# Performance work log

Hardware: AMD Instinct MI355X
Metric: run time of the kernel (lower is better)

## Reference

```python
import jax, jax.numpy as jnp
from jax import lax
import numpy as np

# Module hyperparameters (init_kwargs)
NITERS = 10
NROWS, NCOLS = 16, 16
NSUP = NROWS * NCOLS
COMPACT = 10.0
CONST = 100.0
NCONV = 10  # stage1_nconv; also nfeat of imfeat and shifter_size
B, H, W = 2, 512, 512

DN = ('NCHW', 'OIHW', 'NCHW')


def conv2d(x, w, b=None):
    y = lax.conv_general_dilated(x, w, (1, 1), 'SAME', dimension_numbers=DN)
    return y if b is None else y + b[None, :, None, None]


def blockmean(x):
    # adaptive_avg_pool2d to (NROWS, NCOLS); H,W chosen divisible -> exact block mean
    Bz, C, Hx, Wx = x.shape
    return x.reshape(Bz, C, NROWS, Hx // NROWS, NCOLS, Wx // NCOLS).mean((3, 5))


def box3(x):
    # 3x3 all-ones depthwise conv with zero padding (the "shifter" conv)
    C = x.shape[1]
    k = jnp.ones((C, 1, 3, 3), x.dtype)
    return lax.conv_general_dilated(x, k, (1, 1), 'SAME', feature_group_count=C,
                                    dimension_numbers=DN)


def setup_inputs() -> dict:
    key = jax.random.key(0)
    ks = jax.random.split(key, 7)
    s = 0.15  # ~He init for 3x3 convs with ~10 channels; keeps activations O(1)
    return {
        'X': jax.random.normal(ks[0], (B, 3, H, W), jnp.float32),
        'w0': jax.random.normal(ks[1], (NCONV, 3, 3, 3), jnp.float32) * s,
        'b0': jax.random.normal(ks[2], (NCONV,), jnp.float32) * s,
        'ws_mid': jax.random.normal(ks[3], (NCONV - 2, NCONV, NCONV, 3, 3), jnp.float32) * s,
        'bs_mid': jax.random.normal(ks[4], (NCONV - 2, NCONV), jnp.float32) * s,
        'wf': jax.random.normal(ks[5], (NCONV - 5, NCONV, 3, 3), jnp.float32) * s,
        'bf': jax.random.normal(ks[6], (NCONV - 5,), jnp.float32) * s,
    }


def _forward(X, w0, b0, ws_mid, bs_mid, wf, bf):
    Bz, _, Hx, Wx = X.shape
    h = jax.nn.relu(conv2d(X, w0, b0))

    def layer(hc, wb):
        w, b = wb
        return jax.nn.relu(conv2d(hc, w, b)), None

    h, _ = lax.scan(layer, h, (ws_mid, bs_mid))
    s1 = conv2d(h, wf, bf)  # B x (NCONV-5) x H x W

    # ---- imfeat = [stage1, X, Xgrid, Ygrid] -> B x NCONV x H x W ----
    Yg, Xg = jnp.meshgrid(jnp.arange(Hx, dtype=X.dtype), jnp.arange(Wx, dtype=X.dtype),
                          indexing='ij')
    imfeat = jnp.concatenate([
        s1, X,
        jnp.broadcast_to(Xg, (Bz, 1, Hx, Wx)),
        jnp.broadcast_to(Yg, (Bz, 1, Hx, Wx)),
    ], axis=1)
    C = imfeat.shape[1]

    # ckern: ones, except spatial (last two) channels weighted by compactness scale
    ck = jnp.ones((C,), imfeat.dtype).at[-2:].set(
        jnp.asarray(COMPACT / np.sqrt(Hx * Wx / NSUP), imfeat.dtype))

    # pixel -> parent superpixel indices (nearest-neighbor upsample of coarse grid)
    Yc = jnp.arange(Hx) * NROWS // Hx  # (H,)
    Xc = jnp.arange(Wx) * NCOLS // Wx  # (W,)
    shifts = [(dr, dc) for dr in (-1, 0, 1) for dc in (-1, 0, 1)]
    Y1 = jnp.stack([jnp.clip(Yc + dr, 0, NROWS - 1) for dr, _ in shifts])[:, :, None]  # (9,H,1)
    X1 = jnp.stack([jnp.clip(Xc + dc, 0, NCOLS - 1) for _, dc in shifts])[:, None, :]  # (9,1,W)

    def affinity_fn(cent):
        cup = cent[:, :, Y1, X1]
        d = (imfeat[:, :, None] - cup) * ck[None, :, None, None, None]
        return jnp.exp(-(d * d).mean(1) / CONST)

    def centroids_fn(aff):
        # sum over the 9 shifts commutes with block-mean and the shared 3x3 box conv
        asum = aff.sum(1, keepdims=True)
        num = box3(blockmean(imfeat * asum))  # B x C x NROWS x NCOLS
        den = box3(blockmean(asum))
        return num / den

    cent0 = blockmean(imfeat)
    aff0 = affinity_fn(cent0)

    @jax.checkpoint
    def step(carry, _):
        cent, _a = carry
        aff = affinity_fn(cent)
        return (centroids_fn(aff), aff), None

    (cent, aff), _ = lax.scan(step, (cent0, aff0), None, length=NITERS)
    # returned affinity corresponds to centroids before the last update (as in torch)
    return cent, aff


def reference(X, w0, b0, ws_mid, bs_mid, wf, bf):
    return _forward(X, w0, b0, ws_mid, bs_mid, wf, bf)
```

## Files before the change

kernel.cpp:

```cpp
#include <hip/hip_runtime.h>

#define HH 512
#define WW 512
#define BB 2
#define CKXY 0.3125f
#define HW (HH*WW)

typedef short bf16x8 __attribute__((ext_vector_type(8)));
typedef float f32x4  __attribute__((ext_vector_type(4)));

__device__ __forceinline__ unsigned short f2bf(float f) {
  unsigned u = __float_as_uint(f);
  u += 0x7FFF + ((u >> 16) & 1);
  return (unsigned short)(u >> 16);
}

__global__ __launch_bounds__(512) void conv_mfma(const float* __restrict__ in,
    const float* __restrict__ w, const float* __restrict__ bias,
    float* __restrict__ out) {
  const int bx = blockIdx.x, by = blockIdx.y, b = blockIdx.z;
  const int tid = threadIdx.x;
  const int gy0 = by * 32, gx0 = bx * 32;
  __shared__ unsigned short sT[34 * 34 * 16];
  const float* inb = in + (size_t)b * 10 * HW;

  const int lane = tid & 63;
  const int g = lane >> 4;
  const int co = lane & 15;
  bf16x8 Bf[5];
  #pragma unroll
  for (int P = 0; P < 5; ++P) {
    #pragma unroll
    for (int j = 0; j < 8; ++j) {
      const int tap = 2 * P + (g >> 1);
      const int ci = ((g & 1) << 3) + j;
      unsigned short v = 0;
      if (co < 10 && ci < 10 && tap < 9)
        v = f2bf(w[(co * 10 + ci) * 9 + tap]);
      Bf[P][j] = (short)v;
    }
  }
  const float bs = (co < 10) ? bias[co] : 0.f;

  for (int p = tid; p < 34 * 34; p += 512) {
    const int ly = p / 34, lx = p - ly * 34;
    const int gy = gy0 + ly - 1, gx = gx0 + lx - 1;
    const bool ok = ((unsigned)gy < HH) && ((unsigned)gx < WW);
    const float* pp = inb + gy * WW + gx;
    unsigned u[5];
    #pragma unroll
    for (int c2 = 0; c2 < 5; ++c2) {
      float f0 = ok ? pp[(2 * c2) * HW] : 0.f;
      float f1 = ok ? pp[(2 * c2 + 1) * HW] : 0.f;
      u[c2] = (unsigned)f2bf(f0) | ((unsigned)f2bf(f1) << 16);
    }
    uint4* dst = reinterpret_cast<uint4*>(&sT[p * 16]);
    dst[0] = make_uint4(u[0], u[1], u[2], u[3]);
    dst[1] = make_uint4(u[4], 0u, 0u, 0u);
  }
  __syncthreads();

  const int wave = tid >> 6;
  float* outb = out + (size_t)b * 10 * HW;
  for (int i = 0; i < 8; ++i) {
    const int t = wave * 8 + i;
    const int py = t >> 1;
    const int pxb = (t & 1) << 4;
    f32x4 acc = {bs, bs, bs, bs};
    #pragma unroll
    for (int P = 0; P < 5; ++P) {
      int tap = 2 * P + (g >> 1);
      if (tap > 8) tap = 8;
      const int dy = tap / 3 - 1, dx = tap % 3 - 1;
      const int m = lane & 15;
      const int addr = ((py + 1 + dy) * 34 + (pxb + m + 1 + dx)) * 16 + ((g & 1) << 3);
      bf16x8 a = *reinterpret_cast<const bf16x8*>(&sT[addr]);
      acc = __builtin_amdgcn_mfma_f32_16x16x32_bf16(a, Bf[P], acc, 0, 0, 0);
    }
    if (co < 10) {
      const int y = gy0 + py;
      const int x = gx0 + pxb + (g << 2);
      float4 o;
      o.x = fmaxf(acc[0], 0.f);
      o.y = fmaxf(acc[1], 0.f);
      o.z = fmaxf(acc[2], 0.f);
      o.w = fmaxf(acc[3], 0.f);
      *reinterpret_cast<float4*>(&outb[co * HW + y * WW + x]) = o;
    }
  }
}

template<int CIN, int COUT, bool RELU>
__global__ __launch_bounds__(1024) void conv3x3_t32(const float* __restrict__ in,
    const float* __restrict__ w, const float* __restrict__ bias,
    float* __restrict__ out) {
  const int bx = blockIdx.x, by = blockIdx.y, b = blockIdx.z;
  const int tid = threadIdx.x;
  const int xl = tid & 31, yl = tid >> 5;
  __shared__ float sIn[CIN][34][40];
  const float* inb = in + (size_t)b * CIN * HW;
  const int gy0 = by * 32, gx0 = bx * 32;
  #pragma unroll
  for (int ci = 0; ci < CIN; ++ci)
    sIn[ci][yl + 1][xl + 1] = inb[ci * HW + (gy0 + yl) * WW + gx0 + xl];
  for (int idx = tid; idx < CIN * 132; idx += 1024) {
    int ci = idx / 132, rem = idx - ci * 132;
    int ly, lx;
    if (rem < 34)       { ly = 0;  lx = rem; }
    else if (rem < 68)  { ly = 33; lx = rem - 34; }
    else if (rem < 100) { lx = 0;  ly = rem - 68 + 1; }
    else                { lx = 33; ly = rem - 100 + 1; }
    int gy = gy0 + ly - 1, gx = gx0 + lx - 1;
    float v = 0.f;
    if ((unsigned)gy < HH && (unsigned)gx < WW) v = inb[ci * HW + gy * WW + gx];
    sIn[ci][ly][lx] = v;
  }
  __syncthreads();

  float acc[COUT];
  #pragma unroll
  for (int co = 0; co < COUT; ++co) acc[co] = bias[co];
  #pragma unroll
  for (int ci = 0; ci < CIN; ++ci) {
    float v[9];
    #pragma unroll
    for (int t = 0; t < 9; ++t) v[t] = sIn[ci][yl + t / 3][xl + t % 3];
    #pragma unroll
    for (int co = 0; co < COUT; ++co) {
      #pragma unroll
      for (int t = 0; t < 9; ++t)
        acc[co] = fmaf(v[t], w[(co * CIN + ci) * 9 + t], acc[co]);
    }
  }
  float* outb = out + (size_t)b * COUT * HW;
  const int p = (gy0 + yl) * WW + gx0 + xl;
  #pragma unroll
  for (int co = 0; co < COUT; ++co) {
    float r = RELU ? fmaxf(acc[co], 0.f) : acc[co];
    outb[co * HW + p] = r;
  }
}

__global__ __launch_bounds__(1024) void conv_final_t32(const float* __restrict__ in,
    const float* __restrict__ w, const float* __restrict__ bias,
    const float* __restrict__ X, float* __restrict__ imfeat,
    float* __restrict__ cent0) {
  const int bx = blockIdx.x, by = blockIdx.y, b = blockIdx.z;
  const int tid = threadIdx.x;
  const int xl = tid & 31, yl = tid >> 5;
  __shared__ float sIn[10][34][40];
  const float* inb = in + (size_t)b * 10 * HW;
  const int gy0 = by * 32, gx0 = bx * 32;
  #pragma unroll
  for (int ci = 0; ci < 10; ++ci)
    sIn[ci][yl + 1][xl + 1] = inb[ci * HW + (gy0 + yl) * WW + gx0 + xl];
  for (int idx = tid; idx < 10 * 132; idx += 1024) {
    int ci = idx / 132, rem = idx - ci * 132;
    int ly, lx;
    if (rem < 34)       { ly = 0;  lx = rem; }
    else if (rem < 68)  { ly = 33; lx = rem - 34; }
    else if (rem < 100) { lx = 0;  ly = rem - 68 + 1; }
    else                { lx = 33; ly = rem - 100 + 1; }
    int gy = gy0 + ly - 1, gx = gx0 + lx - 1;
    float v = 0.f;
    if ((unsigned)gy < HH && (unsigned)gx < WW) v = inb[ci * HW + gy * WW + gx];
    sIn[ci][ly][lx] = v;
  }
  __syncthreads();

  float acc[5];
  #pragma unroll
  for (int co = 0; co < 5; ++co) acc[co] = bias[co];
  #pragma unroll
  for (int ci = 0; ci < 10; ++ci) {
    float v[9];
    #pragma unroll
    for (int t = 0; t < 9; ++t) v[t] = sIn[ci][yl + t / 3][xl + t % 3];
    #pragma unroll
    for (int co = 0; co < 5; ++co) {
      #pragma unroll
      for (int t = 0; t < 9; ++t)
        acc[co] = fmaf(v[t], w[(co * 10 + ci) * 9 + t], acc[co]);
    }
  }
  float* ob = imfeat + (size_t)b * 10 * HW;
  const float* Xb = X + (size_t)b * 3 * HW;
  const int y = gy0 + yl, x = gx0 + xl;
  const int p = y * WW + x;
  float cs[10];
  #pragma unroll
  for (int co = 0; co < 5; ++co) { float v = acc[co]; ob[co * HW + p] = v; cs[co] = v; }
  #pragma unroll
  for (int c = 0; c < 3; ++c) { float v = Xb[c * HW + p]; ob[(5 + c) * HW + p] = v; cs[5 + c] = v; }
  float xc = (float)x * CKXY, yc = (float)y * CKXY;
  ob[8 * HW + p] = xc; cs[8] = xc;
  ob[9 * HW + p] = yc; cs[9] = yc;
  #pragma unroll
  for (int off = 32; off; off >>= 1) {
    #pragma unroll
    for (int ch = 0; ch < 10; ++ch) cs[ch] += __shfl_down(cs[ch], off);
  }
  __shared__ float sP[16][10];
  const int wave = tid >> 6;
  if ((tid & 63) == 0) {
    #pragma unroll
    for (int ch = 0; ch < 10; ++ch) sP[wave][ch] = cs[ch];
  }
  __syncthreads();
  if (tid < 10) {
    float s = 0.f;
    #pragma unroll
    for (int wv = 0; wv < 16; ++wv) s += sP[wv][tid];
    cent0[((b * 10 + tid) * 16 + by) * 16 + bx] = s * (1.0f / 1024.0f);
  }
}

__global__ __launch_bounds__(256) void iter2(const float* __restrict__ imfeat,
    const float* __restrict__ centIn, const float* __restrict__ numP,
    const float* __restrict__ denP, float* __restrict__ numO,
    float* __restrict__ denO, float* __restrict__ affO) {
  const int cx = blockIdx.x, cy = blockIdx.y, b = blockIdx.z;
  const int tid = threadIdx.x;
  __shared__ float sc[9][10];
  __shared__ float nb[9][11];
  if (centIn) {
    if (tid < 90) {
      int s = tid / 10, ch = tid - s * 10;
      int dr = s / 3 - 1, dc = s % 3 - 1;
      int r = min(max(cy + dr, 0), 15), c = min(max(cx + dc, 0), 15);
      sc[s][ch] = centIn[((b * 10 + ch) * 16 + r) * 16 + c];
    }
    __syncthreads();
  } else {
    if (tid < 99) {
      int s = tid / 11, j = tid - s * 11;
      int dr = s / 3 - 1, dc = s % 3 - 1;
      int r = min(max(cy + dr, 0), 15), c = min(max(cx + dc, 0), 15);
      float a = 0.f;
      #pragma unroll
      for (int rr = -1; rr <= 1; ++rr)
        #pragma unroll
        for (int cc = -1; cc <= 1; ++cc) {
          int R = r + rr, C = c + cc;
          if ((unsigned)R < 16u && (unsigned)C < 16u)
            a += (j < 10) ? numP[((b * 10 + j) * 16 + R) * 16 + C]
                          : denP[(b * 16 + R) * 16 + C];
        }
      nb[s][j] = a;
    }
    __syncthreads();
    if (tid < 90) {
      int s = tid / 10, ch = tid - s * 10;
      sc[s][ch] = nb[s][ch] / nb[s][10];
    }
    __syncthreads();
  }

  float accN[10];
  #pragma unroll
  for (int ch = 0; ch < 10; ++ch) accN[ch] = 0.f;
  float accD = 0.f;
  const int col = tid & 31, row0 = tid >> 5;
  for (int p = 0; p < 4; ++p) {
    const int y = cy * 32 + row0 + p * 8;
    const int x = cx * 32 + col;
    float f[10];
    #pragma unroll
    for (int ch = 0; ch < 10; ++ch)
      f[ch] = imfeat[((b * 10 + ch) * HH + y) * WW + x];
    float asum = 0.f;
    #pragma unroll
    for (int s = 0; s < 9; ++s) {
      float ss = 0.f;
      #pragma unroll
      for (int ch = 0; ch < 10; ++ch) { float d = f[ch] - sc[s][ch]; ss = fmaf(d, d, ss); }
      float a = __expf(-ss * (1.0f / 1000.0f));
      asum += a;
      if (affO) affO[((b * 9 + s) * HH + y) * WW + x] = a;
    }
    accD += asum;
    #pragma unroll
    for (int ch = 0; ch < 10; ++ch) accN[ch] = fmaf(f[ch], asum, accN[ch]);
  }
  #pragma unroll
  for (int off = 32; off; off >>= 1) {
    accD += __shfl_down(accD, off);
    #pragma unroll
    for (int ch = 0; ch < 10; ++ch) accN[ch] += __shfl_down(accN[ch], off);
  }
  __shared__ float sPart[4][11];
  const int wave = tid >> 6, lane = tid & 63;
  if (lane == 0) {
    #pragma unroll
    for (int ch = 0; ch < 10; ++ch) sPart[wave][ch] = accN[ch];
    sPart[wave][10] = accD;
  }
  __syncthreads();
  if (tid < 11) {
    float s = sPart[0][tid] + sPart[1][tid] + sPart[2][tid] + sPart[3][tid];
    if (tid < 10) numO[((b * 10 + tid) * 16 + cy) * 16 + cx] = s;
    else denO[(b * 16 + cy) * 16 + cx] = s;
  }
}

__global__ __launch_bounds__(256) void cent_final(const float* __restrict__ num_bs,
    const float* __restrict__ den_bs, float* __restrict__ out_cent) {
  const int b = blockIdx.x;
  const int tid = threadIdx.x;
  const int cy = tid >> 4, cx = tid & 15;
  float den = 0.f;
  #pragma unroll
  for (int dr = -1; dr <= 1; ++dr)
    #pragma unroll
    for (int dc = -1; dc <= 1; ++dc) {
      int r = cy + dr, c = cx + dc;
      if ((unsigned)r < 16 && (unsigned)c < 16) den += den_bs[(b * 16 + r) * 16 + c];
    }
  #pragma unroll
  for (int ch = 0; ch < 10; ++ch) {
    float num = 0.f;
    #pragma unroll
    for (int dr = -1; dr <= 1; ++dr)
      #pragma unroll
      for (int dc = -1; dc <= 1; ++dc) {
        int r = cy + dr, c = cx + dc;
        if ((unsigned)r < 16 && (unsigned)c < 16)
          num += num_bs[((b * 10 + ch) * 16 + r) * 16 + c];
      }
    float invck = (ch >= 8) ? (1.0f / CKXY) : 1.0f;
    out_cent[((b * 10 + ch) * 16 + cy) * 16 + cx] = (num / den) * invck;
  }
}

extern "C" void kernel_launch(void* const* d_in, const int* in_sizes, int n_in,
                              void* d_out, int out_size, void* d_ws, size_t ws_size,
                              hipStream_t stream) {
  const float* X      = (const float*)d_in[0];
  const float* w0     = (const float*)d_in[1];
  const float* b0     = (const float*)d_in[2];
  const float* ws_mid = (const float*)d_in[3];
  const float* bs_mid = (const float*)d_in[4];
  const float* wf     = (const float*)d_in[5];
  const float* bf     = (const float*)d_in[6];
  float* out = (float*)d_out;

  const size_t plane = (size_t)BB * 10 * HW;
  float* bufA  = (float*)d_ws;
  float* bufB  = bufA + plane;
  float* num0  = bufB + plane;
  float* den0  = num0 + BB * 10 * 256;
  float* num1  = den0 + BB * 256;
  float* den1  = num1 + BB * 10 * 256;
  float* centA = den1 + BB * 256;

  dim3 cgrid(16, 16, BB);
  conv3x3_t32<3, 10, true><<<cgrid, 1024, 0, stream>>>(X, w0, b0, bufA);
  const float* cur = bufA;
  float* nxt = bufB;
  for (int l = 0; l < 8; ++l) {
    conv_mfma<<<cgrid, 512, 0, stream>>>(cur, ws_mid + l * 900, bs_mid + l * 10, nxt);
    const float* t = cur; cur = nxt; nxt = (float*)t;
  }
  conv_final_t32<<<cgrid, 1024, 0, stream>>>(cur, wf, bf, X, bufB, centA);

  float* aff_out = out + BB * 10 * 256;
  float* nums[2] = {num0, num1};
  float* dens[2] = {den0, den1};
  for (int k = 0; k < 10; ++k) {
    iter2<<<cgrid, 256, 0, stream>>>(bufB,
        (k == 0) ? centA : nullptr,
        (k == 0) ? nullptr : nums[(k - 1) & 1],
        (k == 0) ? nullptr : dens[(k - 1) & 1],
        nums[k & 1], dens[k & 1],
        (k == 9) ? aff_out : nullptr);
  }
  cent_final<<<dim3(BB), 256, 0, stream>>>(nums[1], dens[1], out);
}
```

Before: 291.5 us.

## Store intermediate conv activations as packed bf16 and use MFMA for first/final convs

Intermediate CNN activations are now stored as channel-pair-packed bf16 words instead of fp32, which halves global traffic between the conv layers and removes per-layer fp32-to-bf16 conversion on load. The first 3-channel conv and the final 5-output conv now use the same MFMA tile kernel instead of scalar FMA kernels. Centroid init for the coordinate channels is computed analytically. Output pairs are combined with lane shuffles before packed stores. Rounding to bf16 between layers was already effectively happening, so accuracy risk is small.

```diff
diff --git a/kernel.cpp b/kernel.cpp
--- a/kernel.cpp
+++ b/kernel.cpp
@@ -14,15 +14,18 @@
   u += 0x7FFF + ((u >> 16) & 1);
   return (unsigned short)(u >> 16);
 }
-
-__global__ __launch_bounds__(512) void conv_mfma(const float* __restrict__ in,
+__device__ __forceinline__ unsigned pack2(float lo, float hi) {
+  return (unsigned)f2bf(lo) | ((unsigned)f2bf(hi) << 16);
+}
+
+template<int CIN, bool BF16IN, bool RELU>
+__global__ __launch_bounds__(512) void conv_mfma_u(const void* __restrict__ in,
     const float* __restrict__ w, const float* __restrict__ bias,
-    float* __restrict__ out) {
+    unsigned* __restrict__ outu) {
   const int bx = blockIdx.x, by = blockIdx.y, b = blockIdx.z;
   const int tid = threadIdx.x;
   const int gy0 = by * 32, gx0 = bx * 32;
   __shared__ unsigned short sT[34 * 34 * 16];
-  const float* inb = in + (size_t)b * 10 * HW;
 
   const int lane = tid & 63;
   const int g = lane >> 4;
@@ -35,8 +38,8 @@
       const int tap = 2 * P + (g >> 1);
       const int ci = ((g & 1) << 3) + j;
       unsigned short v = 0;
-      if (co < 10 && ci < 10 && tap < 9)
-        v = f2bf(w[(co * 10 + ci) * 9 + tap]);
+      if (co < 10 && ci < CIN && tap < 9)
+        v = f2bf(w[(co * CIN + ci) * 9 + tap]);
       Bf[P][j] = (short)v;
     }
   }
@@ -46,22 +49,30 @@
     const int ly = p / 34, lx = p - ly * 34;
     const int gy = gy0 + ly - 1, gx = gx0 + lx - 1;
     const bool ok = ((unsigned)gy < HH) && ((unsigned)gx < WW);
-    const float* pp = inb + gy * WW + gx;
-    unsigned u[5];
-    #pragma unroll
-    for (int c2 = 0; c2 < 5; ++c2) {
-      float f0 = ok ? pp[(2 * c2) * HW] : 0.f;
-      float f1 = ok ? pp[(2 * c2 + 1) * HW] : 0.f;
-      u[c2] = (unsigned)f2bf(f0) | ((unsigned)f2bf(f1) << 16);
+    const int pix = gy * WW + gx;
+    unsigned u[8];
+    if (BF16IN) {
+      const unsigned* pp = (const unsigned*)in + (size_t)b * 5 * HW + pix;
+      #pragma unroll
+      for (int c2 = 0; c2 < 8; ++c2)
+        u[c2] = (c2 < (CIN + 1) / 2 && ok) ? pp[c2 * HW] : 0u;
+    } else {
+      const float* pp = (const float*)in + (size_t)b * CIN * HW + pix;
+      #pragma unroll
+      for (int c2 = 0; c2 < 8; ++c2) {
+        float f0 = (2 * c2 < CIN && ok) ? pp[(2 * c2) * HW] : 0.f;
+        float f1 = (2 * c2 + 1 < CIN && ok) ? pp[(2 * c2 + 1) * HW] : 0.f;
+        u[c2] = pack2(f0, f1);
+      }
     }
     uint4* dst = reinterpret_cast<uint4*>(&sT[p * 16]);
     dst[0] = make_uint4(u[0], u[1], u[2], u[3]);
-    dst[1] = make_uint4(u[4], 0u, 0u, 0u);
+    dst[1] = make_uint4(u[4], u[5], u[6], u[7]);
   }
   __syncthreads();
 
   const int wave = tid >> 6;
-  float* outb = out + (size_t)b * 10 * HW;
+  unsigned* ob = outu + (size_t)b * 5 * HW;
   for (int i = 0; i < 8; ++i) {
     const int t = wave * 8 + i;
     const int py = t >> 1;
@@ -77,142 +88,133 @@
       bf16x8 a = *reinterpret_cast<const bf16x8*>(&sT[addr]);
       acc = __builtin_amdgcn_mfma_f32_16x16x32_bf16(a, Bf[P], acc, 0, 0, 0);
     }
-    if (co < 10) {
+    float o0 = acc[0], o1 = acc[1], o2 = acc[2], o3 = acc[3];
+    if (RELU) { o0 = fmaxf(o0, 0.f); o1 = fmaxf(o1, 0.f); o2 = fmaxf(o2, 0.f); o3 = fmaxf(o3, 0.f); }
+    const float q0 = __shfl_xor(o0, 1), q1 = __shfl_xor(o1, 1);
+    const float q2 = __shfl_xor(o2, 1), q3 = __shfl_xor(o3, 1);
+    if (!(co & 1) && co < 10) {
       const int y = gy0 + py;
       const int x = gx0 + pxb + (g << 2);
-      float4 o;
-      o.x = fmaxf(acc[0], 0.f);
-      o.y = fmaxf(acc[1], 0.f);
-      o.z = fmaxf(acc[2], 0.f);
-      o.w = fmaxf(acc[3], 0.f);
-      *reinterpret_cast<float4*>(&outb[co * HW + y * WW + x]) = o;
-    }
-  }
-}
-
-template<int CIN, int COUT, bool RELU>
-__global__ __launch_bounds__(1024) void conv3x3_t32(const float* __restrict__ in,
-    const float* __restrict__ w, const float* __restrict__ bias,
-    float* __restrict__ out) {
-  const int bx = blockIdx.x, by = blockIdx.y, b = blockIdx.z;
-  const int tid = threadIdx.x;
-  const int xl = tid & 31, yl = tid >> 5;
-  __shared__ float sIn[CIN][34][40];
-  const float* inb = in + (size_t)b * CIN * HW;
-  const int gy0 = by * 32, gx0 = bx * 32;
-  #pragma unroll
-  for (int ci = 0; ci < CIN; ++ci)
-    sIn[ci][yl + 1][xl + 1] = inb[ci * HW + (gy0 + yl) * WW + gx0 + xl];
-  for (int idx = tid; idx < CIN * 132; idx += 1024) {
-    int ci = idx / 132, rem = idx - ci * 132;
-    int ly, lx;
-    if (rem < 34)       { ly = 0;  lx = rem; }
-    else if (rem < 68)  { ly = 33; lx = rem - 34; }
-    else if (rem < 100) { lx = 0;  ly = rem - 68 + 1; }
-    else                { lx = 33; ly = rem - 100 + 1; }
-    int gy = gy0 + ly - 1, gx = gx0 + lx - 1;
-    float v = 0.f;
-    if ((unsigned)gy < HH && (unsigned)gx < WW) v = inb[ci * HW + gy * WW + gx];
-    sIn[ci][ly][lx] = v;
-  }
-  __syncthreads();
-
-  float acc[COUT];
-  #pragma unroll
-  for (int co = 0; co < COUT; ++co) acc[co] = bias[co];
-  #pragma unroll
-  for (int ci = 0; ci < CIN; ++ci) {
-    float v[9];
-    #pragma unroll
-    for (int t = 0; t < 9; ++t) v[t] = sIn[ci][yl + t / 3][xl + t % 3];
-    #pragma unroll
-    for (int co = 0; co < COUT; ++co) {
-      #pragma unroll
-      for (int t = 0; t < 9; ++t)
-        acc[co] = fmaf(v[t], w[(co * CIN + ci) * 9 + t], acc[co]);
-    }
-  }
-  float* outb = out + (size_t)b * COUT * HW;
-  const int p = (gy0 + yl) * WW + gx0 + xl;
-  #pragma unroll
-  for (int co = 0; co < COUT; ++co) {
-    float r = RELU ? fmaxf(acc[co], 0.f) : acc[co];
-    outb[co * HW + p] = r;
-  }
-}
-
-__global__ __launch_bounds__(1024) void conv_final_t32(const float* __restrict__ in,
+      uint4 st;
+      st.x = pack2(o0, q0); st.y = pack2(o1, q1);
+      st.z = pack2(o2, q2); st.w = pack2(o3, q3);
+      *reinterpret_cast<uint4*>(&ob[(co >> 1) * HW + y * WW + x]) = st;
+    }
+  }
+}
+
+__global__ __launch_bounds__(512) void conv_final_mfma(const unsigned* __restrict__ in,
     const float* __restrict__ w, const float* __restrict__ bias,
     const float* __restrict__ X, float* __restrict__ imfeat,
     float* __restrict__ cent0) {
   const int bx = blockIdx.x, by = blockIdx.y, b = blockIdx.z;
   const int tid = threadIdx.x;
-  const int xl = tid & 31, yl = tid >> 5;
-  __shared__ float sIn[10][34][40];
-  const float* inb = in + (size_t)b * 10 * HW;
   const int gy0 = by * 32, gx0 = bx * 32;
-  #pragma unroll
-  for (int ci = 0; ci < 10; ++ci)
-    sIn[ci][yl + 1][xl + 1] = inb[ci * HW + (gy0 + yl) * WW + gx0 + xl];
-  for (int idx = tid; idx < 10 * 132; idx += 1024) {
-    int ci = idx / 132, rem = idx - ci * 132;
-    int ly, lx;
-    if (rem < 34)       { ly = 0;  lx = rem; }
-    else if (rem < 68)  { ly = 33; lx = rem - 34; }
-    else if (rem < 100) { lx = 0;  ly = rem - 68 + 1; }
-    else                { lx = 33; ly = rem - 100 + 1; }
-    int gy = gy0 + ly - 1, gx = gx0 + lx - 1;
-    float v = 0.f;
-    if ((unsigned)gy < HH && (unsigned)gx < WW) v = inb[ci * HW + gy * WW + gx];
-    sIn[ci][ly][lx] = v;
+  __shared__ unsigned short sT[34 * 34 * 16];
+  __shared__ float sC[8][5];
+  __shared__ float sX[8][3];
+
+  const int lane = tid & 63;
+  const int g = lane >> 4;
+  const int co = lane & 15;
+  bf16x8 Bf[5];
+  #pragma unroll
+  for (int P = 0; P < 5; ++P) {
+    #pragma unroll
+    for (int j = 0; j < 8; ++j) {
+      const int tap = 2 * P + (g >> 1);
+      const int ci = ((g & 1) << 3) + j;
+      unsigned short v = 0;
+      if (co < 5 && ci < 10 && tap < 9)
+        v = f2bf(w[(co * 10 + ci) * 9 + tap]);
+      Bf[P][j] = (short)v;
+    }
+  }
+  const float bs = (co < 5) ? bias[co] : 0.f;
+
+  for (int p = tid; p < 34 * 34; p += 512) {
+    const int ly = p / 34, lx = p - ly * 34;
+    const int gy = gy0 + ly - 1, gx = gx0 + lx - 1;
+    const bool ok = ((unsigned)gy < HH) && ((unsigned)gx < WW);
+    const unsigned* pp = in + (size_t)b * 5 * HW + gy * WW + gx;
+    unsigned u[5];
+    #pragma unroll
+    for (int c2 = 0; c2 < 5; ++c2) u[c2] = ok ? pp[c2 * HW] : 0u;
+    uint4* dst = reinterpret_cast<uint4*>(&sT[p * 16]);
+    dst[0] = make_uint4(u[0], u[1], u[2], u[3]);
+    dst[1] = make_uint4(u[4], 0u, 0u, 0u);
   }
   __syncthreads();
 
-  float acc[5];
-  #pragma unroll
-  for (int co = 0; co < 5; ++co) acc[co] = bias[co];
-  #pragma unroll
-  for (int ci = 0; ci < 10; ++ci) {
-    float v[9];
-    #pragma unroll
-    for (int t = 0; t < 9; ++t) v[t] = sIn[ci][yl + t / 3][xl + t % 3];
-    #pragma unroll
-    for (int co = 0; co < 5; ++co) {
-      #pragma unroll
-      for (int t = 0; t < 9; ++t)
-        acc[co] = fmaf(v[t], w[(co * 10 + ci) * 9 + t], acc[co]);
-    }
-  }
+  const int wave = tid >> 6;
   float* ob = imfeat + (size_t)b * 10 * HW;
+  float cSum = 0.f;
+  for (int i = 0; i < 8; ++i) {
+    const int t = wave * 8 + i;
+    const int py = t >> 1;
+    const int pxb = (t & 1) << 4;
+    f32x4 acc = {bs, bs, bs, bs};
+    #pragma unroll
+    for (int P = 0; P < 5; ++P) {
+      int tap = 2 * P + (g >> 1);
+      if (tap > 8) tap = 8;
+      const int dy = tap / 3 - 1, dx = tap % 3 - 1;
+      const int m = lane & 15;
+      const int addr = ((py + 1 + dy) * 34 + (pxb + m + 1 + dx)) * 16 + ((g & 1) << 3);
+      bf16x8 a = *reinterpret_cast<const bf16x8*>(&sT[addr]);
+      acc = __builtin_amdgcn_mfma_f32_16x16x32_bf16(a, Bf[P], acc, 0, 0, 0);
+    }
+    if (co < 5) {
+      const int y = gy0 + py;
+      const int x = gx0 + pxb + (g << 2);
+      float4 o; o.x = acc[0]; o.y = acc[1]; o.z = acc[2]; o.w = acc[3];
+      *reinterpret_cast<float4*>(&ob[co * HW + y * WW + x]) = o;
+    }
+    cSum += acc[0] + acc[1] + acc[2] + acc[3];
+  }
+  cSum += __shfl_xor(cSum, 16);
+  cSum += __shfl_xor(cSum, 32);
+  if (lane < 5) sC[wave][lane] = cSum;
+
   const float* Xb = X + (size_t)b * 3 * HW;
-  const int y = gy0 + yl, x = gx0 + xl;
-  const int p = y * WW + x;
-  float cs[10];
-  #pragma unroll
-  for (int co = 0; co < 5; ++co) { float v = acc[co]; ob[co * HW + p] = v; cs[co] = v; }
-  #pragma unroll
-  for (int c = 0; c < 3; ++c) { float v = Xb[c * HW + p]; ob[(5 + c) * HW + p] = v; cs[5 + c] = v; }
-  float xc = (float)x * CKXY, yc = (float)y * CKXY;
-  ob[8 * HW + p] = xc; cs[8] = xc;
-  ob[9 * HW + p] = yc; cs[9] = yc;
+  float xs[3] = {0.f, 0.f, 0.f};
+  for (int p = tid; p < 1024; p += 512) {
+    const int y = gy0 + (p >> 5), x = gx0 + (p & 31);
+    const int pix = y * WW + x;
+    #pragma unroll
+    for (int c = 0; c < 3; ++c) {
+      float v = Xb[c * HW + pix];
+      ob[(5 + c) * HW + pix] = v;
+      xs[c] += v;
+    }
+    ob[8 * HW + pix] = (float)x * CKXY;
+    ob[9 * HW + pix] = (float)y * CKXY;
+  }
   #pragma unroll
   for (int off = 32; off; off >>= 1) {
     #pragma unroll
-    for (int ch = 0; ch < 10; ++ch) cs[ch] += __shfl_down(cs[ch], off);
-  }
-  __shared__ float sP[16][10];
-  const int wave = tid >> 6;
-  if ((tid & 63) == 0) {
-    #pragma unroll
-    for (int ch = 0; ch < 10; ++ch) sP[wave][ch] = cs[ch];
+    for (int c = 0; c < 3; ++c) xs[c] += __shfl_down(xs[c], off);
+  }
+  if (lane == 0) {
+    #pragma unroll
+    for (int c = 0; c < 3; ++c) sX[wave][c] = xs[c];
   }
   __syncthreads();
-  if (tid < 10) {
+  if (tid < 5) {
     float s = 0.f;
     #pragma unroll
-    for (int wv = 0; wv < 16; ++wv) s += sP[wv][tid];
+    for (int wv = 0; wv < 8; ++wv) s += sC[wv][tid];
     cent0[((b * 10 + tid) * 16 + by) * 16 + bx] = s * (1.0f / 1024.0f);
   }
+  if (tid >= 64 && tid < 67) {
+    const int c = tid - 64;
+    float s = 0.f;
+    #pragma unroll
+    for (int wv = 0; wv < 8; ++wv) s += sX[wv][c];
+    cent0[((b * 10 + 5 + c) * 16 + by) * 16 + bx] = s * (1.0f / 1024.0f);
+  }
+  if (tid == 128) cent0[((b * 10 + 8) * 16 + by) * 16 + bx] = ((float)gx0 + 15.5f) * CKXY;
+  if (tid == 129) cent0[((b * 10 + 9) * 16 + by) * 16 + bx] = ((float)gy0 + 15.5f) * CKXY;
 }
 
 __global__ __launch_bounds__(256) void iter2(const float* __restrict__ imfeat,
@@ -344,30 +346,31 @@
   const float* bf     = (const float*)d_in[6];
   float* out = (float*)d_out;
 
-  const size_t plane = (size_t)BB * 10 * HW;
-  float* bufA  = (float*)d_ws;
-  float* bufB  = bufA + plane;
-  float* num0  = bufB + plane;
-  float* den0  = num0 + BB * 10 * 256;
-  float* num1  = den0 + BB * 256;
-  float* den1  = num1 + BB * 10 * 256;
-  float* centA = den1 + BB * 256;
+  const size_t uplane = (size_t)BB * 5 * HW;
+  unsigned* uA   = (unsigned*)d_ws;
+  unsigned* uB   = uA + uplane;
+  float* imfeat  = (float*)(uB + uplane);
+  float* num0    = imfeat + (size_t)BB * 10 * HW;
+  float* den0    = num0 + BB * 10 * 256;
+  float* num1    = den0 + BB * 256;
+  float* den1    = num1 + BB * 10 * 256;
+  float* centA   = den1 + BB * 256;
 
   dim3 cgrid(16, 16, BB);
-  conv3x3_t32<3, 10, true><<<cgrid, 1024, 0, stream>>>(X, w0, b0, bufA);
-  const float* cur = bufA;
-  float* nxt = bufB;
+  conv_mfma_u<3, false, true><<<cgrid, 512, 0, stream>>>(X, w0, b0, uA);
+  const unsigned* cur = uA;
+  unsigned* nxt = uB;
   for (int l = 0; l < 8; ++l) {
-    conv_mfma<<<cgrid, 512, 0, stream>>>(cur, ws_mid + l * 900, bs_mid + l * 10, nxt);
-    const float* t = cur; cur = nxt; nxt = (float*)t;
-  }
-  conv_final_t32<<<cgrid, 1024, 0, stream>>>(cur, wf, bf, X, bufB, centA);
+    conv_mfma_u<10, true, true><<<cgrid, 512, 0, stream>>>(cur, ws_mid + l * 900, bs_mid + l * 10, nxt);
+    const unsigned* t = cur; cur = nxt; nxt = (unsigned*)t;
+  }
+  conv_final_mfma<<<cgrid, 512, 0, stream>>>(cur, wf, bf, X, imfeat, centA);
 
   float* aff_out = out + BB * 10 * 256;
   float* nums[2] = {num0, num1};
   float* dens[2] = {den0, den1};
   for (int k = 0; k < 10; ++k) {
-    iter2<<<cgrid, 256, 0, stream>>>(bufB,
+    iter2<<<cgrid, 256, 0, stream>>>(imfeat,
         (k == 0) ? centA : nullptr,
         (k == 0) ? nullptr : nums[(k - 1) & 1],
         (k == 0) ? nullptr : dens[(k - 1) & 1],
```

New measurement: 255.7 us. 1.14x faster.
